# Kernel tuning notes

Measured on AMD Instinct MI355X. Metric: run time of the kernel, lower is better.

The kernel has to match this reference:

```python
import jax, jax.numpy as jnp
import numpy as np

H = 128          # h_dim
N_NODES = 100000
N_EDGES = 1600000
N_GRAPHS = 256
EPS_BN = 1e-5


def setup_inputs() -> dict:
    key = jax.random.key(0)
    ks = jax.random.split(key, 12)
    x = jax.random.normal(ks[0], (N_NODES, 4), dtype=jnp.float32)
    edge_index = jax.random.randint(ks[1], (2, N_EDGES), 0, N_NODES, dtype=jnp.int64)
    batch = jnp.sort(jax.random.randint(ks[2], (N_NODES,), 0, N_GRAPHS, dtype=jnp.int64))
    # Linear weights (xavier-ish scale), stored as [in, out]
    W1 = jax.random.normal(ks[3], (4, H), dtype=jnp.float32) * (1.0 / np.sqrt(4))
    W2 = jax.random.normal(ks[4], (H, H), dtype=jnp.float32) * (1.0 / np.sqrt(H))
    W3 = jax.random.normal(ks[5], (H, H), dtype=jnp.float32) * (1.0 / np.sqrt(H))
    Wfc = jax.random.normal(ks[6], (H, 1), dtype=jnp.float32) * (1.0 / np.sqrt(H))
    def bn_params(k):
        k1, k2, k3, k4 = jax.random.split(k, 4)
        gamma = 1.0 + 0.1 * jax.random.normal(k1, (H,), dtype=jnp.float32)
        beta = 0.1 * jax.random.normal(k2, (H,), dtype=jnp.float32)
        mean = 0.1 * jax.random.normal(k3, (H,), dtype=jnp.float32)
        var = 1.0 + 0.1 * jax.random.uniform(k4, (H,), dtype=jnp.float32)
        return gamma, beta, mean, var
    g1, b1, m1, v1 = bn_params(ks[7])
    g2, b2, m2, v2 = bn_params(ks[8])
    g3, b3, m3, v3 = bn_params(ks[9])
    return {
        "x": x, "edge_index": edge_index, "batch": batch,
        "W1": W1, "g1": g1, "b1": b1, "m1": m1, "v1": v1,
        "W2": W2, "g2": g2, "b2": b2, "m2": m2, "v2": v2,
        "W3": W3, "g3": g3, "b3": b3, "m3": m3, "v3": v3,
        "Wfc": Wfc,
    }


def _gin_layer(h, src, dst, W, gamma, beta, mean, var):
    # GINConv with eps=0: mlp(x + sum_{j in N(i)} x_j)
    aggr = jax.ops.segment_sum(h[src], dst, num_segments=N_NODES)
    z = (h + aggr) @ W                                  # Linear(bias=False)
    z = (z - mean) * (gamma / jnp.sqrt(var + EPS_BN)) + beta  # BatchNorm1d (eval)
    return jax.nn.relu(z)


def reference(x, edge_index, batch,
              W1, g1, b1, m1, v1,
              W2, g2, b2, m2, v2,
              W3, g3, b3, m3, v3,
              Wfc):
    src, dst = edge_index[0], edge_index[1]
    h = _gin_layer(x, src, dst, W1, g1, b1, m1, v1)
    h = _gin_layer(h, src, dst, W2, g2, b2, m2, v2)
    h = _gin_layer(h, src, dst, W3, g3, b3, m3, v3)
    # dropout: identity in eval mode
    sums = jax.ops.segment_sum(h, batch, num_segments=N_GRAPHS)      # [G, H]
    cnts = jax.ops.segment_sum(jnp.ones((N_NODES, 1), h.dtype), batch,
                               num_segments=N_GRAPHS)                # [G, 1]
    pooled = sums / jnp.maximum(cnts, 1.0)
    return jax.nn.sigmoid(pooled @ Wfc)                               # [G, 1]
```

## Files before the change

kernel.cpp:

```cpp
#include <hip/hip_runtime.h>
#include <hip/hip_fp8.h>
#include <math.h>

#define N_NODES 100000
#define N_EDGES 1600000
#define N_GRAPHS 256
#define H 128
#define EPS_BN 1e-5f
#define ELLW 64

#define PSZ 256
#define PSH 8
#define P_PART 391
#define BLD_NBLK 200
#define EPT 32
#define EPB_A (256 * EPT)

typedef unsigned int uint;
typedef unsigned short ushort;
typedef __attribute__((ext_vector_type(8))) short bf16x8;
typedef __attribute__((ext_vector_type(4))) float f32x4;
typedef __attribute__((ext_vector_type(2))) float f32x2;
typedef __attribute__((ext_vector_type(4))) int i32x4;
typedef __attribute__((ext_vector_type(2))) int i32x2;

__device__ __forceinline__ uint f2bf_bits(float x) {
    uint u = __float_as_uint(x);
    return (u + 0x7fffu + ((u >> 16) & 1u)) >> 16;
}
__device__ __forceinline__ uint pack_bf2(float a, float b) {
    return f2bf_bits(a) | (f2bf_bits(b) << 16);
}

__device__ __forceinline__ unsigned char f32_to_fp8(float x) {
#if __has_builtin(__builtin_amdgcn_cvt_pk_fp8_f32)
    int v = __builtin_amdgcn_cvt_pk_fp8_f32(x, 0.0f, 0, false);
    return (unsigned char)(v & 0xff);
#else
    __hip_fp8_e4m3 q(x);
    return (unsigned char)q.__x;
#endif
}
__device__ __forceinline__ f32x4 fp8x4_to_f32x4(uint v) {
    f32x4 r;
#if __has_builtin(__builtin_amdgcn_cvt_pk_f32_fp8)
    f32x2 lo = __builtin_amdgcn_cvt_pk_f32_fp8((int)v, false);
    f32x2 hi = __builtin_amdgcn_cvt_pk_f32_fp8((int)v, true);
    r.x = lo.x; r.y = lo.y; r.z = hi.x; r.w = hi.y;
#else
    __hip_fp8_e4m3 a, b, c, d;
    a.__x = (unsigned char)(v & 0xff);
    b.__x = (unsigned char)((v >> 8) & 0xff);
    c.__x = (unsigned char)((v >> 16) & 0xff);
    d.__x = (unsigned char)((v >> 24) & 0xff);
    r.x = (float)a; r.y = (float)b; r.z = (float)c; r.w = (float)d;
#endif
    return r;
}

__global__ __launch_bounds__(256) void k_hist(const int* __restrict__ dst,
                                              int* __restrict__ hist,
                                              const int* __restrict__ batch,
                                              int* __restrict__ gstart,
                                              const float* __restrict__ W2,
                                              ushort* __restrict__ Wpk2,
                                              const float* __restrict__ W3,
                                              ushort* __restrict__ Wpk3,
                                              float* __restrict__ Gz,
                                              uint* __restrict__ Hf8pad) {
    __shared__ int h[P_PART];
    int b = blockIdx.x;
    if (b < BLD_NBLK) {
        for (int i = threadIdx.x; i < P_PART; i += 256) h[i] = 0;
        __syncthreads();
        int base = b * EPB_A + threadIdx.x * EPT;
        #pragma unroll
        for (int j = 0; j < EPT / 4; j++) {
            int e = base + j * 4;
            if (e + 4 <= N_EDGES) {
                i32x4 d = __builtin_nontemporal_load((const i32x4*)&dst[e]);
                atomicAdd(&h[d.x >> PSH], 1);
                atomicAdd(&h[d.y >> PSH], 1);
                atomicAdd(&h[d.z >> PSH], 1);
                atomicAdd(&h[d.w >> PSH], 1);
            }
        }
        __syncthreads();
        for (int i = threadIdx.x; i < P_PART; i += 256)
            hist[b * P_PART + i] = h[i];
        return;
    }
    if (b < 592) {
        int n = (b - 200) * 256 + threadIdx.x;
        if (n >= N_NODES) return;
        int g = batch[n];
        int gp = (n == 0) ? -1 : batch[n - 1];
        for (int gr = gp + 1; gr <= g; gr++) gstart[gr] = n;
        if (n == N_NODES - 1) {
            for (int gr = g + 1; gr <= N_GRAPHS; gr++) gstart[gr] = N_NODES;
        }
        return;
    }
    if (b >= 608) {
        if (threadIdx.x < N_GRAPHS) Gz[threadIdx.x] = 0.0f;
        if (threadIdx.x < 32) Hf8pad[threadIdx.x] = 0u;
        return;
    }
    const float* W = (b < 600) ? W2 : W3;
    ushort* Wpk = (b < 600) ? Wpk2 : Wpk3;
    int t = ((b < 600) ? (b - 592) : (b - 600)) * 256 + threadIdx.x;
    int lane = t & 63, nt = (t >> 6) & 7, kt = t >> 9;
    int n = nt * 16 + (lane & 15);
    int kbase = kt * 32 + (lane >> 4) * 8;
    ushort v[8];
    #pragma unroll
    for (int j = 0; j < 8; j++)
        v[j] = (ushort)f2bf_bits(W[(size_t)(kbase + j) * H + n]);
    uint4 pk;
    pk.x = (uint)v[0] | ((uint)v[1] << 16);
    pk.y = (uint)v[2] | ((uint)v[3] << 16);
    pk.z = (uint)v[4] | ((uint)v[5] << 16);
    pk.w = (uint)v[6] | ((uint)v[7] << 16);
    *(uint4*)&Wpk[(size_t)t * 8] = pk;
}

__global__ __launch_bounds__(256) void k_scan_a(const int* __restrict__ hist,
                                                int* __restrict__ offs,
                                                int* __restrict__ tot) {
    __shared__ int lds[256];
    int p = blockIdx.x;
    int t = threadIdx.x;
    int v = (t < BLD_NBLK) ? hist[t * P_PART + p] : 0;
    lds[t] = v;
    __syncthreads();
    for (int off = 1; off < 256; off <<= 1) {
        int tmp = (t >= off) ? lds[t - off] : 0;
        __syncthreads();
        lds[t] += tmp;
        __syncthreads();
    }
    if (t < BLD_NBLK) offs[t * P_PART + p] = lds[t] - v;
    if (t == 255) tot[p] = lds[255];
}

__global__ void k_scan_b(const int* __restrict__ tot, int* __restrict__ parr) {
    __shared__ int lds[512];
    int p = threadIdx.x;
    int v = (p < P_PART) ? tot[p] : 0;
    lds[p] = v;
    __syncthreads();
    for (int off = 1; off < 512; off <<= 1) {
        int tmp = (p >= off) ? lds[p - off] : 0;
        __syncthreads();
        lds[p] += tmp;
        __syncthreads();
    }
    if (p < P_PART) parr[p] = lds[p] - v;
    if (p == 0) parr[P_PART] = N_EDGES;
}

__global__ __launch_bounds__(256) void k_scatter(const int* __restrict__ src,
                                                 const int* __restrict__ dst,
                                                 const int* __restrict__ offs,
                                                 const int* __restrict__ parr,
                                                 i32x2* __restrict__ ebuf) {
    __shared__ int lofs[P_PART];
    for (int i = threadIdx.x; i < P_PART; i += 256)
        lofs[i] = offs[blockIdx.x * P_PART + i] + parr[i];
    __syncthreads();
    int base = blockIdx.x * EPB_A + threadIdx.x * EPT;
    #pragma unroll
    for (int j = 0; j < EPT / 4; j++) {
        int e = base + j * 4;
        if (e + 4 <= N_EDGES) {
            i32x4 d = __builtin_nontemporal_load((const i32x4*)&dst[e]);
            i32x4 s = __builtin_nontemporal_load((const i32x4*)&src[e]);
            #pragma unroll
            for (int k = 0; k < 4; k++) {
                int dk = (k == 0) ? d.x : (k == 1) ? d.y : (k == 2) ? d.z : d.w;
                int sk = (k == 0) ? s.x : (k == 1) ? s.y : (k == 2) ? s.z : s.w;
                int pos = atomicAdd(&lofs[dk >> PSH], 1);
                i32x2 sd; sd.x = sk; sd.y = dk;
                ebuf[pos] = sd;
            }
        }
    }
}

__global__ __launch_bounds__(256) void k_build(const i32x2* __restrict__ ebuf,
                                               const int* __restrict__ parr,
                                               int* __restrict__ cnt,
                                               int* __restrict__ ell) {
    __shared__ int lc[PSZ];
    int p = blockIdx.x;
    for (int i = threadIdx.x; i < PSZ; i += 256) lc[i] = 0;
    __syncthreads();
    int e0 = parr[p], e1 = parr[p + 1];
    for (int i = e0 + threadIdx.x; i < e1; i += 256) {
        i32x2 sd = ebuf[i];
        int d = sd.y;
        int slot = atomicAdd(&lc[d & (PSZ - 1)], 1);
        if (slot < ELLW) ell[(size_t)d * ELLW + slot] = sd.x;
    }
    __syncthreads();
    int nb = p * PSZ;
    for (int i = threadIdx.x; i < PSZ; i += 256) {
        int n = nb + i;
        if (n < N_NODES) {
            int c = lc[i];
            cnt[n] = c;
            int cc = (c < ELLW) ? c : ELLW;
            int cp = (cc + 15) & ~15;
            if (cp > ELLW) cp = ELLW;
            for (int slot = cc; slot < cp; slot++)
                ell[(size_t)n * ELLW + slot] = N_NODES;
        }
    }
}

__global__ __launch_bounds__(256) void k_layer1(
    const float* __restrict__ x, const int* __restrict__ cnt,
    const int* __restrict__ ell, const float* __restrict__ W1,
    const float* __restrict__ gamma, const float* __restrict__ beta,
    const float* __restrict__ mean, const float* __restrict__ var,
    uint* __restrict__ Hf8) {
    __shared__ float scs[128], shs[128];
    int tid = threadIdx.x;
    if (tid < 128) {
        float sc = gamma[tid] * rsqrtf(var[tid] + EPS_BN);
        scs[tid] = sc;
        shs[tid] = beta[tid] - mean[tid] * sc;
    }
    __syncthreads();
    int lane = tid & 63, wave = tid >> 6;
    int sub = lane >> 4, m = lane & 15;
    int n = blockIdx.x * 16 + wave * 4 + sub;
    if (n >= N_NODES) return;
    int cn = cnt[n]; if (cn > ELLW) cn = ELLW;
    const int* row = &ell[(size_t)n * ELLW];
    float4 acc = {0.f, 0.f, 0.f, 0.f};
    for (int e = m; e < cn; e += 16) {
        float4 v = *(const float4*)&x[(size_t)row[e] * 4];
        acc.x += v.x; acc.y += v.y; acc.z += v.z; acc.w += v.w;
    }
    #pragma unroll
    for (int off = 8; off > 0; off >>= 1) {
        acc.x += __shfl_down(acc.x, off, 16);
        acc.y += __shfl_down(acc.y, off, 16);
        acc.z += __shfl_down(acc.z, off, 16);
        acc.w += __shfl_down(acc.w, off, 16);
    }
    int src = lane & 48;
    float4 xs = *(const float4*)&x[(size_t)n * 4];
    float uu[4];
    uu[0] = __shfl(acc.x, src, 64) + xs.x;
    uu[1] = __shfl(acc.y, src, 64) + xs.y;
    uu[2] = __shfl(acc.z, src, 64) + xs.z;
    uu[3] = __shfl(acc.w, src, 64) + xs.w;
    int j0 = m * 8;
    float z[8] = {0.f, 0.f, 0.f, 0.f, 0.f, 0.f, 0.f, 0.f};
    #pragma unroll
    for (int k = 0; k < 4; k++) {
        float4 wa = *(const float4*)&W1[k * H + j0];
        float4 wb = *(const float4*)&W1[k * H + j0 + 4];
        z[0] += uu[k] * wa.x; z[1] += uu[k] * wa.y;
        z[2] += uu[k] * wa.z; z[3] += uu[k] * wa.w;
        z[4] += uu[k] * wb.x; z[5] += uu[k] * wb.y;
        z[6] += uu[k] * wb.z; z[7] += uu[k] * wb.w;
    }
    #pragma unroll
    for (int i = 0; i < 8; i++)
        z[i] = fmaxf(z[i] * scs[j0 + i] + shs[j0 + i], 0.0f);
    uint2 q;
    q.x = (uint)f32_to_fp8(z[0]) | ((uint)f32_to_fp8(z[1]) << 8)
        | ((uint)f32_to_fp8(z[2]) << 16) | ((uint)f32_to_fp8(z[3]) << 24);
    q.y = (uint)f32_to_fp8(z[4]) | ((uint)f32_to_fp8(z[5]) << 8)
        | ((uint)f32_to_fp8(z[6]) << 16) | ((uint)f32_to_fp8(z[7]) << 24);
    *(uint2*)&Hf8[(size_t)n * 32 + m * 2] = q;
}

__global__ __launch_bounds__(256) void k_aggr128(
    const uint* __restrict__ Hf8, const int* __restrict__ cnt,
    const int* __restrict__ ell, uint* __restrict__ Ubf) {
    int t = blockIdx.x * 256 + threadIdx.x;
    int n = t >> 6, lane = t & 63;
    if (n >= N_NODES) return;
    int g = lane >> 4, c8 = lane & 15;
    const int* row = &ell[(size_t)n * ELLW];
    i32x4 id = *(const i32x4*)(row + 4 * g);
    uint2 sp = {0u, 0u};
    if (g == 0) sp = *(const uint2*)&Hf8[(size_t)n * 32 + c8 * 2];
    int cn = cnt[n]; if (cn > ELLW) cn = ELLW;
    int cnp = (cn + 15) & ~15; if (cnp > ELLW) cnp = ELLW;

    f32x4 A = {0.f, 0.f, 0.f, 0.f};
    f32x4 B = {0.f, 0.f, 0.f, 0.f};
    for (int e = 0; e < cnp; e += 16) {
        i32x4 idn = id;
        if (e + 16 < cnp) idn = *(const i32x4*)(row + e + 16 + 4 * g);
        int s0 = id.x, s1 = id.y, s2 = id.z, s3 = id.w;
        uint2 p0 = *(const uint2*)&Hf8[(size_t)s0 * 32 + c8 * 2];
        uint2 p1 = *(const uint2*)&Hf8[(size_t)s1 * 32 + c8 * 2];
        uint2 p2 = *(const uint2*)&Hf8[(size_t)s2 * 32 + c8 * 2];
        uint2 p3 = *(const uint2*)&Hf8[(size_t)s3 * 32 + c8 * 2];
        f32x4 l0 = fp8x4_to_f32x4(p0.x), h0 = fp8x4_to_f32x4(p0.y);
        f32x4 l1 = fp8x4_to_f32x4(p1.x), h1 = fp8x4_to_f32x4(p1.y);
        f32x4 l2 = fp8x4_to_f32x4(p2.x), h2 = fp8x4_to_f32x4(p2.y);
        f32x4 l3 = fp8x4_to_f32x4(p3.x), h3 = fp8x4_to_f32x4(p3.y);
        A += (l0 + l1) + (l2 + l3);
        B += (h0 + h1) + (h2 + h3);
        id = idn;
    }
    if (g == 0) {
        A += fp8x4_to_f32x4(sp.x);
        B += fp8x4_to_f32x4(sp.y);
    }
    #pragma unroll
    for (int off = 32; off >= 16; off >>= 1) {
        A.x += __shfl_down(A.x, off, 64);
        A.y += __shfl_down(A.y, off, 64);
        A.z += __shfl_down(A.z, off, 64);
        A.w += __shfl_down(A.w, off, 64);
        B.x += __shfl_down(B.x, off, 64);
        B.y += __shfl_down(B.y, off, 64);
        B.z += __shfl_down(B.z, off, 64);
        B.w += __shfl_down(B.w, off, 64);
    }
    if (g == 0) {
        uint4 ov;
        ov.x = pack_bf2(A.x, A.y);
        ov.y = pack_bf2(A.z, A.w);
        ov.z = pack_bf2(B.x, B.y);
        ov.w = pack_bf2(B.z, B.w);
        *(uint4*)&Ubf[(size_t)n * 64 + c8 * 4] = ov;
    }
}

__global__ __launch_bounds__(256) void k_gemm_mfma(
    const uint* __restrict__ Ubf, const uint* __restrict__ Wpk,
    const float* __restrict__ gamma, const float* __restrict__ beta,
    const float* __restrict__ mean, const float* __restrict__ var,
    unsigned char* __restrict__ Hf8,
    const int* __restrict__ batch, const float* __restrict__ Wfc,
    float* __restrict__ Gz, int mode) {
    __shared__ uint lds_u[64 * 68];
    __shared__ float wfc[128];
    __shared__ int bb[64];
    __shared__ float sblk[64];
    int tid = threadIdx.x;
    int row0 = blockIdx.x * 64;
    if (mode == 2) {
        if (tid < 128) wfc[tid] = Wfc[tid];
        if (tid < 64) {
            int rr = row0 + tid;
            bb[tid] = (rr < N_NODES) ? batch[rr] : -1;
        }
    }
    #pragma unroll
    for (int it = 0; it < 4; it++) {
        int r = it * 16 + (tid >> 4);
        int c = (tid & 15) * 4;
        int gr = row0 + r; if (gr >= N_NODES) gr = N_NODES - 1;
        uint4 v = *(const uint4*)&Ubf[(size_t)gr * 64 + c];
        *(uint4*)&lds_u[r * 68 + c] = v;
    }
    __syncthreads();

    int wave = tid >> 6, lane = tid & 63;
    int m = lane & 15, quad = lane >> 4;
    bf16x8 a[4];
    #pragma unroll
    for (int kt = 0; kt < 4; kt++)
        a[kt] = *(const bf16x8*)&lds_u[(wave * 16 + m) * 68 + kt * 16 + quad * 4];

    f32x4 acc[8];
    #pragma unroll
    for (int nt = 0; nt < 8; nt++) acc[nt] = (f32x4){0.f, 0.f, 0.f, 0.f};

    #pragma unroll
    for (int nt = 0; nt < 8; nt++) {
        #pragma unroll
        for (int kt = 0; kt < 4; kt++) {
            bf16x8 b = *(const bf16x8*)&Wpk[((size_t)(kt * 8 + nt) * 64 + lane) * 4];
            acc[nt] = __builtin_amdgcn_mfma_f32_16x16x32_bf16(a[kt], b, acc[nt], 0, 0, 0);
        }
    }

    if (mode == 1) {
        #pragma unroll
        for (int nt = 0; nt < 8; nt++) {
            int col = nt * 16 + m;
            float sc = gamma[col] * rsqrtf(var[col] + EPS_BN);
            float sh = beta[col] - mean[col] * sc;
            #pragma unroll
            for (int r = 0; r < 4; r++) {
                int row = row0 + wave * 16 + quad * 4 + r;
                if (row < N_NODES) {
                    float z = fmaxf(acc[nt][r] * sc + sh, 0.0f);
                    Hf8[(size_t)row * 128 + col] = f32_to_fp8(z);
                }
            }
        }
    } else {
        float pr[4] = {0.f, 0.f, 0.f, 0.f};
        #pragma unroll
        for (int nt = 0; nt < 8; nt++) {
            int col = nt * 16 + m;
            float sc = gamma[col] * rsqrtf(var[col] + EPS_BN);
            float sh = beta[col] - mean[col] * sc;
            float wf = wfc[col];
            #pragma unroll
            for (int r = 0; r < 4; r++) {
                float z = fmaxf(acc[nt][r] * sc + sh, 0.0f);
                pr[r] += z * wf;
            }
        }
        #pragma unroll
        for (int r = 0; r < 4; r++) {
            float p = pr[r];
            p += __shfl_down(p, 8, 16);
            p += __shfl_down(p, 4, 16);
            p += __shfl_down(p, 2, 16);
            p += __shfl_down(p, 1, 16);
            if (m == 0) sblk[wave * 16 + quad * 4 + r] = p;
        }
        __syncthreads();
        if (tid == 0) {
            int i = 0;
            while (i < 64 && row0 + i < N_NODES) {
                int g = bb[i];
                float s = 0.0f;
                while (i < 64 && row0 + i < N_NODES && bb[i] == g) {
                    s += sblk[i]; i++;
                }
                atomicAdd(&Gz[g], s);
            }
        }
    }
}

__global__ void k_fc(const float* __restrict__ Gz, const int* __restrict__ gstart,
                     float* __restrict__ out) {
    int g = threadIdx.x;
    if (g < N_GRAPHS) {
        int c = gstart[g + 1] - gstart[g];
        float z = Gz[g] / fmaxf((float)c, 1.0f);
        out[g] = 1.0f / (1.0f + expf(-z));
    }
}

extern "C" void kernel_launch(void* const* d_in, const int* in_sizes, int n_in,
                              void* d_out, int out_size, void* d_ws, size_t ws_size,
                              hipStream_t stream) {
    const float* x     = (const float*)d_in[0];
    const int*   ei    = (const int*)d_in[1];
    const int*   batch = (const int*)d_in[2];
    const float* W1    = (const float*)d_in[3];
    const float* g1    = (const float*)d_in[4];
    const float* b1    = (const float*)d_in[5];
    const float* m1    = (const float*)d_in[6];
    const float* v1    = (const float*)d_in[7];
    const float* W2    = (const float*)d_in[8];
    const float* g2    = (const float*)d_in[9];
    const float* b2    = (const float*)d_in[10];
    const float* m2    = (const float*)d_in[11];
    const float* v2    = (const float*)d_in[12];
    const float* W3    = (const float*)d_in[13];
    const float* g3    = (const float*)d_in[14];
    const float* b3    = (const float*)d_in[15];
    const float* m3    = (const float*)d_in[16];
    const float* v3    = (const float*)d_in[17];
    const float* Wfc   = (const float*)d_in[18];
    float* out = (float*)d_out;

    const int* srcp = ei;
    const int* dstp = ei + N_EDGES;

    uint* Ubf  = (uint*)d_ws;
    uint* Hf8u = Ubf + (size_t)N_NODES * 64;
    int* cnt   = (int*)(Hf8u + (size_t)N_NODES * 32 + 32);
    int* ell   = cnt + N_NODES;
    int* gstart = ell + (size_t)N_NODES * ELLW;
    ushort* Wpk2 = (ushort*)(gstart + 260);
    ushort* Wpk3 = Wpk2 + 16384;
    int* hist  = (int*)(Wpk3 + 16384);
    int* offs  = hist + BLD_NBLK * P_PART;
    int* parr  = offs + BLD_NBLK * P_PART;
    int* tot   = parr + 400;
    float* Gz  = (float*)(tot + 400);
    i32x2* ebuf = (i32x2*)Ubf;
    uint* Hf8pad = Hf8u + (size_t)N_NODES * 32;

    k_hist<<<609, 256, 0, stream>>>(dstp, hist, batch, gstart, W2, Wpk2, W3, Wpk3,
                                    Gz, Hf8pad);
    k_scan_a<<<P_PART, 256, 0, stream>>>(hist, offs, tot);
    k_scan_b<<<1, 512, 0, stream>>>(tot, parr);
    k_scatter<<<BLD_NBLK, 256, 0, stream>>>(srcp, dstp, offs, parr, ebuf);
    k_build<<<P_PART, 256, 0, stream>>>(ebuf, parr, cnt, ell);

    k_layer1<<<(N_NODES + 15) / 16, 256, 0, stream>>>(
        x, cnt, ell, W1, g1, b1, m1, v1, Hf8u);
    k_aggr128<<<(N_NODES * 64 + 255) / 256, 256, 0, stream>>>(Hf8u, cnt, ell, Ubf);
    k_gemm_mfma<<<(N_NODES + 63) / 64, 256, 0, stream>>>(
        Ubf, (const uint*)Wpk2, g2, b2, m2, v2, (unsigned char*)Hf8u,
        batch, Wfc, Gz, 1);
    k_aggr128<<<(N_NODES * 64 + 255) / 256, 256, 0, stream>>>(Hf8u, cnt, ell, Ubf);
    k_gemm_mfma<<<(N_NODES + 63) / 64, 256, 0, stream>>>(
        Ubf, (const uint*)Wpk3, g3, b3, m3, v3, (unsigned char*)Hf8u,
        batch, Wfc, Gz, 2);
    k_fc<<<1, 256, 0, stream>>>(Gz, gstart, out);
}
```

Before: 278.0 us.

## Fuse neighbor aggregation into the MFMA GEMM kernel with ping-pong feature buffers

Merges the separate aggregation and GEMM kernels for layers 2 and 3 into one kernel. Each wave gathers and sums neighbor features for its 16 rows and writes the bf16 result straight into LDS, instead of round-tripping the aggregated features through global memory. The fused kernel reads from one fp8 feature buffer and writes to the other (HfA/HfB), since updating in place would race with other blocks still gathering. This removes one launch per layer and the global write and reread of the aggregated features. The cost is that each wave now walks 16 nodes one after another, leaving fewer independent waves to hide gather latency.

After: 287.2 us. +3.3%, slower.

```diff
diff --git a/kernel.cpp b/kernel.cpp
--- a/kernel.cpp
+++ b/kernel.cpp
@@ -67,7 +67,8 @@
                                               const float* __restrict__ W3,
                                               ushort* __restrict__ Wpk3,
                                               float* __restrict__ Gz,
-                                              uint* __restrict__ Hf8pad) {
+                                              uint* __restrict__ HfApad,
+                                              uint* __restrict__ HfBpad) {
     __shared__ int h[P_PART];
     int b = blockIdx.x;
     if (b < BLD_NBLK) {
@@ -103,7 +104,8 @@
     }
     if (b >= 608) {
         if (threadIdx.x < N_GRAPHS) Gz[threadIdx.x] = 0.0f;
-        if (threadIdx.x < 32) Hf8pad[threadIdx.x] = 0u;
+        if (threadIdx.x < 32) HfApad[threadIdx.x] = 0u;
+        if (threadIdx.x < 32) HfBpad[threadIdx.x] = 0u;
         return;
     }
     const float* W = (b < 600) ? W2 : W3;
@@ -279,68 +281,12 @@
     *(uint2*)&Hf8[(size_t)n * 32 + m * 2] = q;
 }
 
-__global__ __launch_bounds__(256) void k_aggr128(
-    const uint* __restrict__ Hf8, const int* __restrict__ cnt,
-    const int* __restrict__ ell, uint* __restrict__ Ubf) {
-    int t = blockIdx.x * 256 + threadIdx.x;
-    int n = t >> 6, lane = t & 63;
-    if (n >= N_NODES) return;
-    int g = lane >> 4, c8 = lane & 15;
-    const int* row = &ell[(size_t)n * ELLW];
-    i32x4 id = *(const i32x4*)(row + 4 * g);
-    uint2 sp = {0u, 0u};
-    if (g == 0) sp = *(const uint2*)&Hf8[(size_t)n * 32 + c8 * 2];
-    int cn = cnt[n]; if (cn > ELLW) cn = ELLW;
-    int cnp = (cn + 15) & ~15; if (cnp > ELLW) cnp = ELLW;
-
-    f32x4 A = {0.f, 0.f, 0.f, 0.f};
-    f32x4 B = {0.f, 0.f, 0.f, 0.f};
-    for (int e = 0; e < cnp; e += 16) {
-        i32x4 idn = id;
-        if (e + 16 < cnp) idn = *(const i32x4*)(row + e + 16 + 4 * g);
-        int s0 = id.x, s1 = id.y, s2 = id.z, s3 = id.w;
-        uint2 p0 = *(const uint2*)&Hf8[(size_t)s0 * 32 + c8 * 2];
-        uint2 p1 = *(const uint2*)&Hf8[(size_t)s1 * 32 + c8 * 2];
-        uint2 p2 = *(const uint2*)&Hf8[(size_t)s2 * 32 + c8 * 2];
-        uint2 p3 = *(const uint2*)&Hf8[(size_t)s3 * 32 + c8 * 2];
-        f32x4 l0 = fp8x4_to_f32x4(p0.x), h0 = fp8x4_to_f32x4(p0.y);
-        f32x4 l1 = fp8x4_to_f32x4(p1.x), h1 = fp8x4_to_f32x4(p1.y);
-        f32x4 l2 = fp8x4_to_f32x4(p2.x), h2 = fp8x4_to_f32x4(p2.y);
-        f32x4 l3 = fp8x4_to_f32x4(p3.x), h3 = fp8x4_to_f32x4(p3.y);
-        A += (l0 + l1) + (l2 + l3);
-        B += (h0 + h1) + (h2 + h3);
-        id = idn;
-    }
-    if (g == 0) {
-        A += fp8x4_to_f32x4(sp.x);
-        B += fp8x4_to_f32x4(sp.y);
-    }
-    #pragma unroll
-    for (int off = 32; off >= 16; off >>= 1) {
-        A.x += __shfl_down(A.x, off, 64);
-        A.y += __shfl_down(A.y, off, 64);
-        A.z += __shfl_down(A.z, off, 64);
-        A.w += __shfl_down(A.w, off, 64);
-        B.x += __shfl_down(B.x, off, 64);
-        B.y += __shfl_down(B.y, off, 64);
-        B.z += __shfl_down(B.z, off, 64);
-        B.w += __shfl_down(B.w, off, 64);
-    }
-    if (g == 0) {
-        uint4 ov;
-        ov.x = pack_bf2(A.x, A.y);
-        ov.y = pack_bf2(A.z, A.w);
-        ov.z = pack_bf2(B.x, B.y);
-        ov.w = pack_bf2(B.z, B.w);
-        *(uint4*)&Ubf[(size_t)n * 64 + c8 * 4] = ov;
-    }
-}
-
-__global__ __launch_bounds__(256) void k_gemm_mfma(
-    const uint* __restrict__ Ubf, const uint* __restrict__ Wpk,
+__global__ __launch_bounds__(256) void k_aggr_gemm(
+    const uint* __restrict__ Hin, const int* __restrict__ cnt,
+    const int* __restrict__ ell, const uint* __restrict__ Wpk,
     const float* __restrict__ gamma, const float* __restrict__ beta,
     const float* __restrict__ mean, const float* __restrict__ var,
-    unsigned char* __restrict__ Hf8,
+    unsigned char* __restrict__ Hout,
     const int* __restrict__ batch, const float* __restrict__ Wfc,
     float* __restrict__ Gz, int mode) {
     __shared__ uint lds_u[64 * 68];
@@ -356,18 +302,77 @@
             bb[tid] = (rr < N_NODES) ? batch[rr] : -1;
         }
     }
-    #pragma unroll
-    for (int it = 0; it < 4; it++) {
-        int r = it * 16 + (tid >> 4);
-        int c = (tid & 15) * 4;
-        int gr = row0 + r; if (gr >= N_NODES) gr = N_NODES - 1;
-        uint4 v = *(const uint4*)&Ubf[(size_t)gr * 64 + c];
-        *(uint4*)&lds_u[r * 68 + c] = v;
-    }
-    __syncthreads();
-
     int wave = tid >> 6, lane = tid & 63;
-    int m = lane & 15, quad = lane >> 4;
+    int g = lane >> 4, c8 = lane & 15;
+    int n0 = row0 + wave * 16;
+
+    int cnt16 = 0;
+    if (lane < 16) {
+        int nn = n0 + lane;
+        cnt16 = (nn < N_NODES) ? cnt[nn] : 0;
+    }
+    int npre = (n0 < N_NODES) ? n0 : (N_NODES - 1);
+    i32x4 idp = *(const i32x4*)(ell + (size_t)npre * ELLW + 4 * g);
+
+    for (int i = 0; i < 16; i++) {
+        int n = n0 + i;
+        bool valid = (n < N_NODES);
+        int cn = __shfl(cnt16, i, 64);
+        if (cn > ELLW) cn = ELLW;
+        int cnp = (cn + 15) & ~15;
+        const int* row = ell + (size_t)(valid ? n : (N_NODES - 1)) * ELLW;
+        i32x4 id = idp;
+        if (i < 15) {
+            int n2 = n + 1; if (n2 >= N_NODES) n2 = N_NODES - 1;
+            idp = *(const i32x4*)(ell + (size_t)n2 * ELLW + 4 * g);
+        }
+        uint2 sp = {0u, 0u};
+        if (g == 0 && valid) sp = *(const uint2*)&Hin[(size_t)n * 32 + c8 * 2];
+
+        f32x4 A = {0.f, 0.f, 0.f, 0.f};
+        f32x4 B = {0.f, 0.f, 0.f, 0.f};
+        for (int e = 0; e < cnp; e += 16) {
+            i32x4 idn = id;
+            if (e + 16 < cnp) idn = *(const i32x4*)(row + e + 16 + 4 * g);
+            int s0 = id.x, s1 = id.y, s2 = id.z, s3 = id.w;
+            uint2 p0 = *(const uint2*)&Hin[(size_t)s0 * 32 + c8 * 2];
+            uint2 p1 = *(const uint2*)&Hin[(size_t)s1 * 32 + c8 * 2];
+            uint2 p2 = *(const uint2*)&Hin[(size_t)s2 * 32 + c8 * 2];
+            uint2 p3 = *(const uint2*)&Hin[(size_t)s3 * 32 + c8 * 2];
+            f32x4 l0 = fp8x4_to_f32x4(p0.x), h0 = fp8x4_to_f32x4(p0.y);
+            f32x4 l1 = fp8x4_to_f32x4(p1.x), h1 = fp8x4_to_f32x4(p1.y);
+            f32x4 l2 = fp8x4_to_f32x4(p2.x), h2 = fp8x4_to_f32x4(p2.y);
+            f32x4 l3 = fp8x4_to_f32x4(p3.x), h3 = fp8x4_to_f32x4(p3.y);
+            A += (l0 + l1) + (l2 + l3);
+            B += (h0 + h1) + (h2 + h3);
+            id = idn;
+        }
+        if (g == 0) {
+            A += fp8x4_to_f32x4(sp.x);
+            B += fp8x4_to_f32x4(sp.y);
+        }
+        #pragma unroll
+        for (int off = 32; off >= 16; off >>= 1) {
+            A.x += __shfl_down(A.x, off, 64);
+            A.y += __shfl_down(A.y, off, 64);
+            A.z += __shfl_down(A.z, off, 64);
+            A.w += __shfl_down(A.w, off, 64);
+            B.x += __shfl_down(B.x, off, 64);
+            B.y += __shfl_down(B.y, off, 64);
+            B.z += __shfl_down(B.z, off, 64);
+            B.w += __shfl_down(B.w, off, 64);
+        }
+        if (g == 0) {
+            uint4 ov;
+            ov.x = pack_bf2(A.x, A.y);
+            ov.y = pack_bf2(A.z, A.w);
+            ov.z = pack_bf2(B.x, B.y);
+            ov.w = pack_bf2(B.z, B.w);
+            *(uint4*)&lds_u[(wave * 16 + i) * 68 + c8 * 4] = ov;
+        }
+    }
+
+    int m = c8, quad = g;
     bf16x8 a[4];
     #pragma unroll
     for (int kt = 0; kt < 4; kt++)
@@ -397,7 +402,7 @@
                 int row = row0 + wave * 16 + quad * 4 + r;
                 if (row < N_NODES) {
                     float z = fmaxf(acc[nt][r] * sc + sh, 0.0f);
-                    Hf8[(size_t)row * 128 + col] = f32_to_fp8(z);
+                    Hout[(size_t)row * 128 + col] = f32_to_fp8(z);
                 }
             }
         }
@@ -428,12 +433,12 @@
         if (tid == 0) {
             int i = 0;
             while (i < 64 && row0 + i < N_NODES) {
-                int g = bb[i];
+                int gg = bb[i];
                 float s = 0.0f;
-                while (i < 64 && row0 + i < N_NODES && bb[i] == g) {
+                while (i < 64 && row0 + i < N_NODES && bb[i] == gg) {
                     s += sblk[i]; i++;
                 }
-                atomicAdd(&Gz[g], s);
+                atomicAdd(&Gz[gg], s);
             }
         }
     }
@@ -476,9 +481,9 @@
     const int* srcp = ei;
     const int* dstp = ei + N_EDGES;
 
-    uint* Ubf  = (uint*)d_ws;
-    uint* Hf8u = Ubf + (size_t)N_NODES * 64;
-    int* cnt   = (int*)(Hf8u + (size_t)N_NODES * 32 + 32);
+    uint* HfB  = (uint*)d_ws;
+    uint* HfA  = HfB + (size_t)N_NODES * 32 + 32;
+    int* cnt   = (int*)(HfA + (size_t)N_NODES * 32 + 32);
     int* ell   = cnt + N_NODES;
     int* gstart = ell + (size_t)N_NODES * ELLW;
     ushort* Wpk2 = (ushort*)(gstart + 260);
@@ -488,25 +493,24 @@
     int* parr  = offs + BLD_NBLK * P_PART;
     int* tot   = parr + 400;
     float* Gz  = (float*)(tot + 400);
-    i32x2* ebuf = (i32x2*)Ubf;
-    uint* Hf8pad = Hf8u + (size_t)N_NODES * 32;
+    i32x2* ebuf = (i32x2*)HfB;
+    uint* HfApad = HfA + (size_t)N_NODES * 32;
+    uint* HfBpad = HfB + (size_t)N_NODES * 32;
 
     k_hist<<<609, 256, 0, stream>>>(dstp, hist, batch, gstart, W2, Wpk2, W3, Wpk3,
-                                    Gz, Hf8pad);
+                                    Gz, HfApad, HfBpad);
     k_scan_a<<<P_PART, 256, 0, stream>>>(hist, offs, tot);
     k_scan_b<<<1, 512, 0, stream>>>(tot, parr);
     k_scatter<<<BLD_NBLK, 256, 0, stream>>>(srcp, dstp, offs, parr, ebuf);
     k_build<<<P_PART, 256, 0, stream>>>(ebuf, parr, cnt, ell);
 
     k_layer1<<<(N_NODES + 15) / 16, 256, 0, stream>>>(
-        x, cnt, ell, W1, g1, b1, m1, v1, Hf8u);
-    k_aggr128<<<(N_NODES * 64 + 255) / 256, 256, 0, stream>>>(Hf8u, cnt, ell, Ubf);
-    k_gemm_mfma<<<(N_NODES + 63) / 64, 256, 0, stream>>>(
-        Ubf, (const uint*)Wpk2, g2, b2, m2, v2, (unsigned char*)Hf8u,
-        batch, Wfc, Gz, 1);
-    k_aggr128<<<(N_NODES * 64 + 255) / 256, 256, 0, stream>>>(Hf8u, cnt, ell, Ubf);
-    k_gemm_mfma<<<(N_NODES + 63) / 64, 256, 0, stream>>>(
-        Ubf, (const uint*)Wpk3, g3, b3, m3, v3, (unsigned char*)Hf8u,
-        batch, Wfc, Gz, 2);
+        x, cnt, ell, W1, g1, b1, m1, v1, HfA);
+    k_aggr_gemm<<<(N_NODES + 63) / 64, 256, 0, stream>>>(
+        HfA, cnt, ell, (const uint*)Wpk2, g2, b2, m2, v2,
+        (unsigned char*)HfB, batch, Wfc, Gz, 1);
+    k_aggr_gemm<<<(N_NODES + 63) / 64, 256, 0, stream>>>(
+        HfB, cnt, ell, (const uint*)Wpk3, g3, b3, m3, v3,
+        (unsigned char*)HfA, batch, Wfc, Gz, 2);
     k_fc<<<1, 256, 0, stream>>>(Gz, gstart, out);
 }
```

## Build ELL adjacency directly with global per-node atomics, dropping partitioned sort

Applied to the files above, without the earlier changes.

The old pipeline built the ELL neighbour table in stages: a partition histogram, two scan kernels, a scatter into an edge buffer, and a per-partition build. It is replaced by one kernel that does a global atomicAdd on each destination node's counter and writes the source straight into its ELL slot. Counter zeroing is folded into the prep kernel, and ELL padding moves into k_layer1. This removes four launches and a full round trip of the edge buffer through memory. In exchange it adds 1.6M random global atomics, and neighbour order inside each row becomes nondeterministic, which changes the summation order.

After: 306.5 us. 1.1x slower.

```diff
diff --git a/kernel.cpp b/kernel.cpp
--- a/kernel.cpp
+++ b/kernel.cpp
@@ -9,9 +9,6 @@
 #define EPS_BN 1e-5f
 #define ELLW 64
 
-#define PSZ 256
-#define PSH 8
-#define P_PART 391
 #define BLD_NBLK 200
 #define EPT 32
 #define EPB_A (256 * EPT)
@@ -22,7 +19,6 @@
 typedef __attribute__((ext_vector_type(4))) float f32x4;
 typedef __attribute__((ext_vector_type(2))) float f32x2;
 typedef __attribute__((ext_vector_type(4))) int i32x4;
-typedef __attribute__((ext_vector_type(2))) int i32x2;
 
 __device__ __forceinline__ uint f2bf_bits(float x) {
     uint u = __float_as_uint(x);
@@ -58,40 +54,18 @@
     return r;
 }
 
-__global__ __launch_bounds__(256) void k_hist(const int* __restrict__ dst,
-                                              int* __restrict__ hist,
-                                              const int* __restrict__ batch,
+__global__ __launch_bounds__(256) void k_prep(const int* __restrict__ batch,
                                               int* __restrict__ gstart,
                                               const float* __restrict__ W2,
                                               ushort* __restrict__ Wpk2,
                                               const float* __restrict__ W3,
                                               ushort* __restrict__ Wpk3,
                                               float* __restrict__ Gz,
-                                              uint* __restrict__ Hf8pad) {
-    __shared__ int h[P_PART];
+                                              uint* __restrict__ Hf8pad,
+                                              int* __restrict__ cnt) {
     int b = blockIdx.x;
-    if (b < BLD_NBLK) {
-        for (int i = threadIdx.x; i < P_PART; i += 256) h[i] = 0;
-        __syncthreads();
-        int base = b * EPB_A + threadIdx.x * EPT;
-        #pragma unroll
-        for (int j = 0; j < EPT / 4; j++) {
-            int e = base + j * 4;
-            if (e + 4 <= N_EDGES) {
-                i32x4 d = __builtin_nontemporal_load((const i32x4*)&dst[e]);
-                atomicAdd(&h[d.x >> PSH], 1);
-                atomicAdd(&h[d.y >> PSH], 1);
-                atomicAdd(&h[d.z >> PSH], 1);
-                atomicAdd(&h[d.w >> PSH], 1);
-            }
-        }
-        __syncthreads();
-        for (int i = threadIdx.x; i < P_PART; i += 256)
-            hist[b * P_PART + i] = h[i];
-        return;
-    }
-    if (b < 592) {
-        int n = (b - 200) * 256 + threadIdx.x;
+    if (b < 392) {
+        int n = b * 256 + threadIdx.x;
         if (n >= N_NODES) return;
         int g = batch[n];
         int gp = (n == 0) ? -1 : batch[n - 1];
@@ -101,73 +75,41 @@
         }
         return;
     }
-    if (b >= 608) {
+    if (b < 408) {
+        const float* W = (b < 400) ? W2 : W3;
+        ushort* Wpk = (b < 400) ? Wpk2 : Wpk3;
+        int t = ((b < 400) ? (b - 392) : (b - 400)) * 256 + threadIdx.x;
+        int lane = t & 63, nt = (t >> 6) & 7, kt = t >> 9;
+        int n = nt * 16 + (lane & 15);
+        int kbase = kt * 32 + (lane >> 4) * 8;
+        ushort v[8];
+        #pragma unroll
+        for (int j = 0; j < 8; j++)
+            v[j] = (ushort)f2bf_bits(W[(size_t)(kbase + j) * H + n]);
+        uint4 pk;
+        pk.x = (uint)v[0] | ((uint)v[1] << 16);
+        pk.y = (uint)v[2] | ((uint)v[3] << 16);
+        pk.z = (uint)v[4] | ((uint)v[5] << 16);
+        pk.w = (uint)v[6] | ((uint)v[7] << 16);
+        *(uint4*)&Wpk[(size_t)t * 8] = pk;
+        return;
+    }
+    if (b == 408) {
         if (threadIdx.x < N_GRAPHS) Gz[threadIdx.x] = 0.0f;
         if (threadIdx.x < 32) Hf8pad[threadIdx.x] = 0u;
         return;
     }
-    const float* W = (b < 600) ? W2 : W3;
-    ushort* Wpk = (b < 600) ? Wpk2 : Wpk3;
-    int t = ((b < 600) ? (b - 592) : (b - 600)) * 256 + threadIdx.x;
-    int lane = t & 63, nt = (t >> 6) & 7, kt = t >> 9;
-    int n = nt * 16 + (lane & 15);
-    int kbase = kt * 32 + (lane >> 4) * 8;
-    ushort v[8];
-    #pragma unroll
-    for (int j = 0; j < 8; j++)
-        v[j] = (ushort)f2bf_bits(W[(size_t)(kbase + j) * H + n]);
-    uint4 pk;
-    pk.x = (uint)v[0] | ((uint)v[1] << 16);
-    pk.y = (uint)v[2] | ((uint)v[3] << 16);
-    pk.z = (uint)v[4] | ((uint)v[5] << 16);
-    pk.w = (uint)v[6] | ((uint)v[7] << 16);
-    *(uint4*)&Wpk[(size_t)t * 8] = pk;
-}
-
-__global__ __launch_bounds__(256) void k_scan_a(const int* __restrict__ hist,
-                                                int* __restrict__ offs,
-                                                int* __restrict__ tot) {
-    __shared__ int lds[256];
-    int p = blockIdx.x;
-    int t = threadIdx.x;
-    int v = (t < BLD_NBLK) ? hist[t * P_PART + p] : 0;
-    lds[t] = v;
-    __syncthreads();
-    for (int off = 1; off < 256; off <<= 1) {
-        int tmp = (t >= off) ? lds[t - off] : 0;
-        __syncthreads();
-        lds[t] += tmp;
-        __syncthreads();
-    }
-    if (t < BLD_NBLK) offs[t * P_PART + p] = lds[t] - v;
-    if (t == 255) tot[p] = lds[255];
-}
-
-__global__ void k_scan_b(const int* __restrict__ tot, int* __restrict__ parr) {
-    __shared__ int lds[512];
-    int p = threadIdx.x;
-    int v = (p < P_PART) ? tot[p] : 0;
-    lds[p] = v;
-    __syncthreads();
-    for (int off = 1; off < 512; off <<= 1) {
-        int tmp = (p >= off) ? lds[p - off] : 0;
-        __syncthreads();
-        lds[p] += tmp;
-        __syncthreads();
-    }
-    if (p < P_PART) parr[p] = lds[p] - v;
-    if (p == 0) parr[P_PART] = N_EDGES;
-}
-
-__global__ __launch_bounds__(256) void k_scatter(const int* __restrict__ src,
-                                                 const int* __restrict__ dst,
-                                                 const int* __restrict__ offs,
-                                                 const int* __restrict__ parr,
-                                                 i32x2* __restrict__ ebuf) {
-    __shared__ int lofs[P_PART];
-    for (int i = threadIdx.x; i < P_PART; i += 256)
-        lofs[i] = offs[blockIdx.x * P_PART + i] + parr[i];
-    __syncthreads();
+    int i = (b - 409) * 1024 + threadIdx.x * 4;
+    if (i + 4 <= N_NODES) {
+        i32x4 z = {0, 0, 0, 0};
+        *(i32x4*)&cnt[i] = z;
+    }
+}
+
+__global__ __launch_bounds__(256) void k_build_direct(const int* __restrict__ src,
+                                                      const int* __restrict__ dst,
+                                                      int* __restrict__ cnt,
+                                                      int* __restrict__ ell) {
     int base = blockIdx.x * EPB_A + threadIdx.x * EPT;
     #pragma unroll
     for (int j = 0; j < EPT / 4; j++) {
@@ -179,48 +121,16 @@
             for (int k = 0; k < 4; k++) {
                 int dk = (k == 0) ? d.x : (k == 1) ? d.y : (k == 2) ? d.z : d.w;
                 int sk = (k == 0) ? s.x : (k == 1) ? s.y : (k == 2) ? s.z : s.w;
-                int pos = atomicAdd(&lofs[dk >> PSH], 1);
-                i32x2 sd; sd.x = sk; sd.y = dk;
-                ebuf[pos] = sd;
+                int slot = atomicAdd(&cnt[dk], 1);
+                if (slot < ELLW) ell[(size_t)dk * ELLW + slot] = sk;
             }
-        }
-    }
-}
-
-__global__ __launch_bounds__(256) void k_build(const i32x2* __restrict__ ebuf,
-                                               const int* __restrict__ parr,
-                                               int* __restrict__ cnt,
-                                               int* __restrict__ ell) {
-    __shared__ int lc[PSZ];
-    int p = blockIdx.x;
-    for (int i = threadIdx.x; i < PSZ; i += 256) lc[i] = 0;
-    __syncthreads();
-    int e0 = parr[p], e1 = parr[p + 1];
-    for (int i = e0 + threadIdx.x; i < e1; i += 256) {
-        i32x2 sd = ebuf[i];
-        int d = sd.y;
-        int slot = atomicAdd(&lc[d & (PSZ - 1)], 1);
-        if (slot < ELLW) ell[(size_t)d * ELLW + slot] = sd.x;
-    }
-    __syncthreads();
-    int nb = p * PSZ;
-    for (int i = threadIdx.x; i < PSZ; i += 256) {
-        int n = nb + i;
-        if (n < N_NODES) {
-            int c = lc[i];
-            cnt[n] = c;
-            int cc = (c < ELLW) ? c : ELLW;
-            int cp = (cc + 15) & ~15;
-            if (cp > ELLW) cp = ELLW;
-            for (int slot = cc; slot < cp; slot++)
-                ell[(size_t)n * ELLW + slot] = N_NODES;
         }
     }
 }
 
 __global__ __launch_bounds__(256) void k_layer1(
     const float* __restrict__ x, const int* __restrict__ cnt,
-    const int* __restrict__ ell, const float* __restrict__ W1,
+    int* __restrict__ ell, const float* __restrict__ W1,
     const float* __restrict__ gamma, const float* __restrict__ beta,
     const float* __restrict__ mean, const float* __restrict__ var,
     uint* __restrict__ Hf8) {
@@ -237,7 +147,11 @@
     int n = blockIdx.x * 16 + wave * 4 + sub;
     if (n >= N_NODES) return;
     int cn = cnt[n]; if (cn > ELLW) cn = ELLW;
-    const int* row = &ell[(size_t)n * ELLW];
+    int* row = &ell[(size_t)n * ELLW];
+    {
+        int cp = (cn + 15) & ~15; if (cp > ELLW) cp = ELLW;
+        for (int s2 = cn + m; s2 < cp; s2 += 16) row[s2] = N_NODES;
+    }
     float4 acc = {0.f, 0.f, 0.f, 0.f};
     for (int e = m; e < cn; e += 16) {
         float4 v = *(const float4*)&x[(size_t)row[e] * 4];
@@ -483,20 +397,12 @@
     int* gstart = ell + (size_t)N_NODES * ELLW;
     ushort* Wpk2 = (ushort*)(gstart + 260);
     ushort* Wpk3 = Wpk2 + 16384;
-    int* hist  = (int*)(Wpk3 + 16384);
-    int* offs  = hist + BLD_NBLK * P_PART;
-    int* parr  = offs + BLD_NBLK * P_PART;
-    int* tot   = parr + 400;
-    float* Gz  = (float*)(tot + 400);
-    i32x2* ebuf = (i32x2*)Ubf;
+    float* Gz  = (float*)(Wpk3 + 16384);
     uint* Hf8pad = Hf8u + (size_t)N_NODES * 32;
 
-    k_hist<<<609, 256, 0, stream>>>(dstp, hist, batch, gstart, W2, Wpk2, W3, Wpk3,
-                                    Gz, Hf8pad);
-    k_scan_a<<<P_PART, 256, 0, stream>>>(hist, offs, tot);
-    k_scan_b<<<1, 512, 0, stream>>>(tot, parr);
-    k_scatter<<<BLD_NBLK, 256, 0, stream>>>(srcp, dstp, offs, parr, ebuf);
-    k_build<<<P_PART, 256, 0, stream>>>(ebuf, parr, cnt, ell);
+    k_prep<<<507, 256, 0, stream>>>(batch, gstart, W2, Wpk2, W3, Wpk3,
+                                    Gz, Hf8pad, cnt);
+    k_build_direct<<<BLD_NBLK, 256, 0, stream>>>(srcp, dstp, cnt, ell);
 
     k_layer1<<<(N_NODES + 15) / 16, 256, 0, stream>>>(
         x, cnt, ell, W1, g1, b1, m1, v1, Hf8u);
```

## Fuse layer-1 aggregation into ELL build kernel and unroll neighbor gather

Applied to the files above, without the earlier changes.

Merges the layer-1 kernel into k_build, so each block builds the ELL rows for its 256-node partition and then computes the first GIN layer for those nodes, reading the counts from shared memory. This drops one kernel launch and the round trip of counts through global memory. The cost is lower parallelism for layer 1: 391 blocks now cover it instead of about 6250, and the ELL rows just written by the same block are read back. It also rewrites the aggr128 gather to load all four index chunks up front and run four guarded gather steps, giving more memory-level parallelism.

Result: slower. 291.1 us (+4.7%).

```diff
diff --git a/kernel.cpp b/kernel.cpp
--- a/kernel.cpp
+++ b/kernel.cpp
@@ -187,16 +187,26 @@
     }
 }
 
-__global__ __launch_bounds__(256) void k_build(const i32x2* __restrict__ ebuf,
-                                               const int* __restrict__ parr,
-                                               int* __restrict__ cnt,
-                                               int* __restrict__ ell) {
+__global__ __launch_bounds__(256) void k_build(
+    const i32x2* __restrict__ ebuf, const int* __restrict__ parr,
+    int* __restrict__ cnt, int* __restrict__ ell,
+    const float* __restrict__ x, const float* __restrict__ W1,
+    const float* __restrict__ gamma, const float* __restrict__ beta,
+    const float* __restrict__ mean, const float* __restrict__ var,
+    uint* __restrict__ Hf8) {
     __shared__ int lc[PSZ];
+    __shared__ float scs[128], shs[128];
     int p = blockIdx.x;
-    for (int i = threadIdx.x; i < PSZ; i += 256) lc[i] = 0;
+    int tid = threadIdx.x;
+    if (tid < 128) {
+        float sc = gamma[tid] * rsqrtf(var[tid] + EPS_BN);
+        scs[tid] = sc;
+        shs[tid] = beta[tid] - mean[tid] * sc;
+    }
+    for (int i = tid; i < PSZ; i += 256) lc[i] = 0;
     __syncthreads();
     int e0 = parr[p], e1 = parr[p + 1];
-    for (int i = e0 + threadIdx.x; i < e1; i += 256) {
+    for (int i = e0 + tid; i < e1; i += 256) {
         i32x2 sd = ebuf[i];
         int d = sd.y;
         int slot = atomicAdd(&lc[d & (PSZ - 1)], 1);
@@ -204,7 +214,7 @@
     }
     __syncthreads();
     int nb = p * PSZ;
-    for (int i = threadIdx.x; i < PSZ; i += 256) {
+    for (int i = tid; i < PSZ; i += 256) {
         int n = nb + i;
         if (n < N_NODES) {
             int c = lc[i];
@@ -216,67 +226,57 @@
                 ell[(size_t)n * ELLW + slot] = N_NODES;
         }
     }
-}
-
-__global__ __launch_bounds__(256) void k_layer1(
-    const float* __restrict__ x, const int* __restrict__ cnt,
-    const int* __restrict__ ell, const float* __restrict__ W1,
-    const float* __restrict__ gamma, const float* __restrict__ beta,
-    const float* __restrict__ mean, const float* __restrict__ var,
-    uint* __restrict__ Hf8) {
-    __shared__ float scs[128], shs[128];
-    int tid = threadIdx.x;
-    if (tid < 128) {
-        float sc = gamma[tid] * rsqrtf(var[tid] + EPS_BN);
-        scs[tid] = sc;
-        shs[tid] = beta[tid] - mean[tid] * sc;
-    }
-    __syncthreads();
+    __syncthreads();
+
     int lane = tid & 63, wave = tid >> 6;
     int sub = lane >> 4, m = lane & 15;
-    int n = blockIdx.x * 16 + wave * 4 + sub;
-    if (n >= N_NODES) return;
-    int cn = cnt[n]; if (cn > ELLW) cn = ELLW;
-    const int* row = &ell[(size_t)n * ELLW];
-    float4 acc = {0.f, 0.f, 0.f, 0.f};
-    for (int e = m; e < cn; e += 16) {
-        float4 v = *(const float4*)&x[(size_t)row[e] * 4];
-        acc.x += v.x; acc.y += v.y; acc.z += v.z; acc.w += v.w;
-    }
-    #pragma unroll
-    for (int off = 8; off > 0; off >>= 1) {
-        acc.x += __shfl_down(acc.x, off, 16);
-        acc.y += __shfl_down(acc.y, off, 16);
-        acc.z += __shfl_down(acc.z, off, 16);
-        acc.w += __shfl_down(acc.w, off, 16);
-    }
-    int src = lane & 48;
-    float4 xs = *(const float4*)&x[(size_t)n * 4];
-    float uu[4];
-    uu[0] = __shfl(acc.x, src, 64) + xs.x;
-    uu[1] = __shfl(acc.y, src, 64) + xs.y;
-    uu[2] = __shfl(acc.z, src, 64) + xs.z;
-    uu[3] = __shfl(acc.w, src, 64) + xs.w;
-    int j0 = m * 8;
-    float z[8] = {0.f, 0.f, 0.f, 0.f, 0.f, 0.f, 0.f, 0.f};
-    #pragma unroll
-    for (int k = 0; k < 4; k++) {
-        float4 wa = *(const float4*)&W1[k * H + j0];
-        float4 wb = *(const float4*)&W1[k * H + j0 + 4];
-        z[0] += uu[k] * wa.x; z[1] += uu[k] * wa.y;
-        z[2] += uu[k] * wa.z; z[3] += uu[k] * wa.w;
-        z[4] += uu[k] * wb.x; z[5] += uu[k] * wb.y;
-        z[6] += uu[k] * wb.z; z[7] += uu[k] * wb.w;
-    }
-    #pragma unroll
-    for (int i = 0; i < 8; i++)
-        z[i] = fmaxf(z[i] * scs[j0 + i] + shs[j0 + i], 0.0f);
-    uint2 q;
-    q.x = (uint)f32_to_fp8(z[0]) | ((uint)f32_to_fp8(z[1]) << 8)
-        | ((uint)f32_to_fp8(z[2]) << 16) | ((uint)f32_to_fp8(z[3]) << 24);
-    q.y = (uint)f32_to_fp8(z[4]) | ((uint)f32_to_fp8(z[5]) << 8)
-        | ((uint)f32_to_fp8(z[6]) << 16) | ((uint)f32_to_fp8(z[7]) << 24);
-    *(uint2*)&Hf8[(size_t)n * 32 + m * 2] = q;
+    for (int pass = 0; pass < 16; pass++) {
+        int li = pass * 16 + wave * 4 + sub;
+        int n = nb + li;
+        if (n < N_NODES) {
+            int cn = lc[li]; if (cn > ELLW) cn = ELLW;
+            const int* row = &ell[(size_t)n * ELLW];
+            float4 acc = {0.f, 0.f, 0.f, 0.f};
+            for (int e = m; e < cn; e += 16) {
+                float4 v = *(const float4*)&x[(size_t)row[e] * 4];
+                acc.x += v.x; acc.y += v.y; acc.z += v.z; acc.w += v.w;
+            }
+            #pragma unroll
+            for (int off = 8; off > 0; off >>= 1) {
+                acc.x += __shfl_down(acc.x, off, 16);
+                acc.y += __shfl_down(acc.y, off, 16);
+                acc.z += __shfl_down(acc.z, off, 16);
+                acc.w += __shfl_down(acc.w, off, 16);
+            }
+            int srcl = lane & 48;
+            float4 xs = *(const float4*)&x[(size_t)n * 4];
+            float uu[4];
+            uu[0] = __shfl(acc.x, srcl, 64) + xs.x;
+            uu[1] = __shfl(acc.y, srcl, 64) + xs.y;
+            uu[2] = __shfl(acc.z, srcl, 64) + xs.z;
+            uu[3] = __shfl(acc.w, srcl, 64) + xs.w;
+            int j0 = m * 8;
+            float z[8] = {0.f, 0.f, 0.f, 0.f, 0.f, 0.f, 0.f, 0.f};
+            #pragma unroll
+            for (int k = 0; k < 4; k++) {
+                float4 wa = *(const float4*)&W1[k * H + j0];
+                float4 wb = *(const float4*)&W1[k * H + j0 + 4];
+                z[0] += uu[k] * wa.x; z[1] += uu[k] * wa.y;
+                z[2] += uu[k] * wa.z; z[3] += uu[k] * wa.w;
+                z[4] += uu[k] * wb.x; z[5] += uu[k] * wb.y;
+                z[6] += uu[k] * wb.z; z[7] += uu[k] * wb.w;
+            }
+            #pragma unroll
+            for (int i = 0; i < 8; i++)
+                z[i] = fmaxf(z[i] * scs[j0 + i] + shs[j0 + i], 0.0f);
+            uint2 q;
+            q.x = (uint)f32_to_fp8(z[0]) | ((uint)f32_to_fp8(z[1]) << 8)
+                | ((uint)f32_to_fp8(z[2]) << 16) | ((uint)f32_to_fp8(z[3]) << 24);
+            q.y = (uint)f32_to_fp8(z[4]) | ((uint)f32_to_fp8(z[5]) << 8)
+                | ((uint)f32_to_fp8(z[6]) << 16) | ((uint)f32_to_fp8(z[7]) << 24);
+            *(uint2*)&Hf8[(size_t)n * 32 + m * 2] = q;
+        }
+    }
 }
 
 __global__ __launch_bounds__(256) void k_aggr128(
@@ -285,32 +285,36 @@
     int t = blockIdx.x * 256 + threadIdx.x;
     int n = t >> 6, lane = t & 63;
     if (n >= N_NODES) return;
+    int cn = cnt[n];
     int g = lane >> 4, c8 = lane & 15;
     const int* row = &ell[(size_t)n * ELLW];
-    i32x4 id = *(const i32x4*)(row + 4 * g);
+    i32x4 id0 = *(const i32x4*)(row + 4 * g);
     uint2 sp = {0u, 0u};
     if (g == 0) sp = *(const uint2*)&Hf8[(size_t)n * 32 + c8 * 2];
-    int cn = cnt[n]; if (cn > ELLW) cn = ELLW;
+    if (cn > ELLW) cn = ELLW;
     int cnp = (cn + 15) & ~15; if (cnp > ELLW) cnp = ELLW;
+    i32x4 id1 = *(const i32x4*)(row + ((cnp > 16) ? 16 : 0) + 4 * g);
+    i32x4 id2 = *(const i32x4*)(row + ((cnp > 32) ? 32 : 0) + 4 * g);
+    i32x4 id3 = *(const i32x4*)(row + ((cnp > 48) ? 48 : 0) + 4 * g);
 
     f32x4 A = {0.f, 0.f, 0.f, 0.f};
     f32x4 B = {0.f, 0.f, 0.f, 0.f};
-    for (int e = 0; e < cnp; e += 16) {
-        i32x4 idn = id;
-        if (e + 16 < cnp) idn = *(const i32x4*)(row + e + 16 + 4 * g);
-        int s0 = id.x, s1 = id.y, s2 = id.z, s3 = id.w;
-        uint2 p0 = *(const uint2*)&Hf8[(size_t)s0 * 32 + c8 * 2];
-        uint2 p1 = *(const uint2*)&Hf8[(size_t)s1 * 32 + c8 * 2];
-        uint2 p2 = *(const uint2*)&Hf8[(size_t)s2 * 32 + c8 * 2];
-        uint2 p3 = *(const uint2*)&Hf8[(size_t)s3 * 32 + c8 * 2];
+    auto gather16 = [&](i32x4 id) {
+        uint2 p0 = *(const uint2*)&Hf8[(size_t)id.x * 32 + c8 * 2];
+        uint2 p1 = *(const uint2*)&Hf8[(size_t)id.y * 32 + c8 * 2];
+        uint2 p2 = *(const uint2*)&Hf8[(size_t)id.z * 32 + c8 * 2];
+        uint2 p3 = *(const uint2*)&Hf8[(size_t)id.w * 32 + c8 * 2];
         f32x4 l0 = fp8x4_to_f32x4(p0.x), h0 = fp8x4_to_f32x4(p0.y);
         f32x4 l1 = fp8x4_to_f32x4(p1.x), h1 = fp8x4_to_f32x4(p1.y);
         f32x4 l2 = fp8x4_to_f32x4(p2.x), h2 = fp8x4_to_f32x4(p2.y);
         f32x4 l3 = fp8x4_to_f32x4(p3.x), h3 = fp8x4_to_f32x4(p3.y);
         A += (l0 + l1) + (l2 + l3);
         B += (h0 + h1) + (h2 + h3);
-        id = idn;
-    }
+    };
+    if (cnp > 0)  gather16(id0);
+    if (cnp > 16) gather16(id1);
+    if (cnp > 32) gather16(id2);
+    if (cnp > 48) gather16(id3);
     if (g == 0) {
         A += fp8x4_to_f32x4(sp.x);
         B += fp8x4_to_f32x4(sp.y);
@@ -496,10 +500,9 @@
     k_scan_a<<<P_PART, 256, 0, stream>>>(hist, offs, tot);
     k_scan_b<<<1, 512, 0, stream>>>(tot, parr);
     k_scatter<<<BLD_NBLK, 256, 0, stream>>>(srcp, dstp, offs, parr, ebuf);
-    k_build<<<P_PART, 256, 0, stream>>>(ebuf, parr, cnt, ell);
-
-    k_layer1<<<(N_NODES + 15) / 16, 256, 0, stream>>>(
-        x, cnt, ell, W1, g1, b1, m1, v1, Hf8u);
+    k_build<<<P_PART, 256, 0, stream>>>(ebuf, parr, cnt, ell,
+                                        x, W1, g1, b1, m1, v1, Hf8u);
+
     k_aggr128<<<(N_NODES * 64 + 255) / 256, 256, 0, stream>>>(Hf8u, cnt, ell, Ubf);
     k_gemm_mfma<<<(N_NODES + 63) / 64, 256, 0, stream>>>(
         Ubf, (const uint*)Wpk2, g2, b2, m2, v2, (unsigned char*)Hf8u,
```
